# Performance work log

Measured on AMD Instinct MI355X. Metric: run time of the kernel, lower is better.

Reference implementation:

```python
import jax, jax.numpy as jnp
import numpy as np

B, S, D, H, F = 8, 1024, 512, 8, 2048
EPS = 1e-3  # keras default for BatchNormalization and LayerNormalization


def _layernorm(x, g, b):
    m = jnp.mean(x, axis=-1, keepdims=True)
    v = jnp.var(x, axis=-1, keepdims=True)
    return (x - m) * jax.lax.rsqrt(v + EPS) * g + b


def setup_inputs() -> dict:
    key = jax.random.key(0)
    ks = jax.random.split(key, 16)
    sc = 0.02
    inp = {
        "Q": jax.random.normal(ks[0], (B, S, D), jnp.float32),
        "K": jax.random.normal(ks[1], (B, S, D), jnp.float32),
        "V": jax.random.normal(ks[2], (B, S, D), jnp.float32),
        # per-head QKV projections stacked: [H, D, D]
        "WQ": jax.random.normal(ks[3], (H, D, D), jnp.float32) * sc,
        "bQ": jnp.zeros((H, D), jnp.float32),
        "WK": jax.random.normal(ks[4], (H, D, D), jnp.float32) * sc,
        "bK": jnp.zeros((H, D), jnp.float32),
        "WV": jax.random.normal(ks[5], (H, D, D), jnp.float32) * sc,
        "bV": jnp.zeros((H, D), jnp.float32),
        "Wo": jax.random.normal(ks[6], (H * D, D), jnp.float32) * sc,
        "bo": jnp.zeros((D,), jnp.float32),
        # FeedForward
        "W0": jax.random.normal(ks[7], (D, F), jnp.float32) * sc,
        "b0": jnp.zeros((F,), jnp.float32),
        "g0": jnp.ones((F,), jnp.float32),
        "be0": jnp.zeros((F,), jnp.float32),
        "m0": jnp.zeros((F,), jnp.float32),   # BN moving mean
        "v0": jnp.ones((F,), jnp.float32),    # BN moving var
        "a0": jnp.zeros((S, F), jnp.float32),  # PReLU alpha (keras default shape/init)
        "W1": jax.random.normal(ks[8], (F, F), jnp.float32) * sc,
        "b1": jnp.zeros((F,), jnp.float32),
        "g1": jnp.ones((F,), jnp.float32),
        "be1": jnp.zeros((F,), jnp.float32),
        "m1": jnp.zeros((F,), jnp.float32),
        "v1": jnp.ones((F,), jnp.float32),
        "a1": jnp.zeros((S, F), jnp.float32),
        "W2": jax.random.normal(ks[9], (F, D), jnp.float32) * sc,
        "b2": jnp.zeros((D,), jnp.float32),
        "ln0g": jnp.ones((D,), jnp.float32),
        "ln0b": jnp.zeros((D,), jnp.float32),
        "ln1g": jnp.ones((D,), jnp.float32),
        "ln1b": jnp.zeros((D,), jnp.float32),
    }
    return inp


def reference(Q, K, V, WQ, bQ, WK, bK, WV, bV, Wo, bo,
              W0, b0, g0, be0, m0, v0, a0,
              W1, b1, g1, be1, m1, v1, a1,
              W2, b2, ln0g, ln0b, ln1g, ln1b):
    # ---- MultiHeadAttention (all heads batched) ----
    qh = jnp.einsum('bsd,hde->bhse', Q, WQ) + bQ[None, :, None, :]
    kh = jnp.einsum('bsd,hde->bhse', K, WK) + bK[None, :, None, :]
    vh = jnp.einsum('bsd,hde->bhse', V, WV) + bV[None, :, None, :]
    # NOTE: source scales by 1/dk, not 1/sqrt(dk)
    scores = jnp.einsum('bhse,bhte->bhst', qh, kh) * (1.0 / D)
    attn = jax.nn.softmax(scores, axis=-1)
    ctx = jnp.einsum('bhst,bhte->bhse', attn, vh)        # [B,H,S,D]
    cat = jnp.transpose(ctx, (0, 2, 1, 3)).reshape(B, S, H * D)
    mha = cat @ Wo + bo
    x = _layernorm(Q + mha, ln0g, ln0b)
    # ---- FeedForward (inference: BN uses moving stats, dropout off) ----
    h0 = x @ W0 + b0
    h0 = (h0 - m0) * jax.lax.rsqrt(v0 + EPS) * g0 + be0
    h0 = jnp.where(h0 > 0, h0, a0 * h0)                   # PReLU
    h1 = h0 @ W1 + b1
    h1 = (h1 - m1) * jax.lax.rsqrt(v1 + EPS) * g1 + be1
    h1 = jnp.where(h1 > 0, h1, a1 * h1)
    ff = h1 @ W2 + b2
    return _layernorm(x + ff, ln1g, ln1b)
```

## Files before the change

### kernel.cpp

```cpp
#include <hip/hip_runtime.h>
#include <hip/hip_bf16.h>
#include <cstdint>
#include <cstddef>

#define Sd 1024
#define Dd 512
#define Hd 8
#define Fd 2048
#define Bd 8
#define EPSf 1e-3f

typedef __bf16 bf16x8 __attribute__((ext_vector_type(8)));
typedef float f32x4 __attribute__((ext_vector_type(4)));
typedef __attribute__((address_space(3))) unsigned int lds_u32;
typedef __attribute__((address_space(1))) const unsigned int gl_u32;

#define BM 128
#define BN 128
#define BK 32

enum { EPI_BF16 = 0, EPI_F32 = 1, EPI_BNPRELU = 2, EPI_SCORES = 3, EPI_PV = 4 };

__device__ __forceinline__ void gl_lds16(const void* g, void* l) {
  __builtin_amdgcn_global_load_lds((gl_u32*)g, (lds_u32*)l, 16, 0, 0);
}


#define LGKM(n)                                                  \
  asm volatile("s_waitcnt lgkmcnt(" #n ")" ::: "memory");        \
  __builtin_amdgcn_sched_barrier(0)
#define VMC(n) asm volatile("s_waitcnt vmcnt(" #n ")" ::: "memory")

#define LDA_(dst, dof, xr, mh)                                               \
  _Pragma("unroll") for (int i_ = 0; i_ < 4; ++i_)                           \
      dst[i_] = *(const bf16x8*)(aw + (dof) + (xr) + (mh) * 8192 + i_ * 2048);
#define LDB_(dst, dof, xr)                                                   \
  _Pragma("unroll") for (int i_ = 0; i_ < 4; ++i_)                           \
      dst[i_] = *(const bf16x8*)(bw + (dof) + (xr) + i_ * 2048);
#define MFMAQ(q, av, bv)                                                     \
  __builtin_amdgcn_s_setprio(1);                                             \
  {                                                                          \
    _Pragma("unroll") for (int i_ = 0; i_ < 4; ++i_) {                       \
      _Pragma("unroll") for (int n_ = 0; n_ < 4; ++n_)                       \
          acc[(q) * 4 + i_][n_] = __builtin_amdgcn_mfma_f32_16x16x32_bf16(   \
              av[i_], bv[n_], acc[(q) * 4 + i_][n_], 0, 0, 0);               \
    }                                                                        \
  }                                                                          \
  __builtin_amdgcn_s_setprio(0)

template <int EPI>
__global__ __launch_bounds__(512, 2) void big_gemm(
    const __hip_bfloat16* __restrict__ A_, int lda, size_t sA1, size_t sA2,
    const __hip_bfloat16* __restrict__ B_, size_t sB1,
    const float* __restrict__ bias_,
    void* __restrict__ C_, int ldc, size_t sC, int K, float alpha,
    const float* __restrict__ bn_g, const float* __restrict__ bn_b,
    const float* __restrict__ bn_m, const float* __restrict__ bn_v,
    const float* __restrict__ pa) {
  __shared__ __align__(16) char lds[131072];
  const int tid = threadIdx.x;
  const int gx = gridDim.x;
  const int nwg = gx * gridDim.y;
  const int orig = blockIdx.y * gx + blockIdx.x;
  const int wgid = (orig & 7) * (nwg >> 3) + (orig >> 3);
  const int bx = wgid % gx;
  const int by = wgid / gx;
  const int m0 = by * 256, n0 = bx * 256;
  const int z = blockIdx.z;
  const int z1 = z >> 3, z2 = z & 7;

  const int lane = tid & 63;
  const int wid = tid >> 6;
  const int wm = wid >> 2;
  const int wn = wid & 3;
  const int fr = lane & 15;
  const int kg = lane >> 4;

  const int r0 = tid >> 3;
  const int c0 = (tid & 7) ^ (r0 & 7);
  const size_t lda2 = (size_t)lda * 2;
  const size_t ldb2 = (size_t)K * 2;
  const char* Ab = (const char*)(A_ + (size_t)z1 * sA1 + (size_t)z2 * sA2) +
                   (size_t)(m0 + r0) * lda2 + c0 * 16;
  const char* Bb = (const char*)(B_ + (size_t)z1 * sB1) + (size_t)(n0 + r0) * ldb2 + c0 * 16;

  const int axor0 = (kg ^ (fr & 7)) << 4;
  const int axor1 = ((4 + kg) ^ (fr & 7)) << 4;
  const char* aw = lds + (wm << 14) + fr * 128;
  const char* bw = lds + 32768 + ((wn >> 1) << 14) + ((wn & 1) << 13) + fr * 128;

  auto STG = [&](int nof, int H, int u) {
    char* L = lds + nof + (H << 14) + tid * 16;
    const size_t rs = (H < 2) ? lda2 : ldb2;
    const char* src = ((H < 2) ? Ab : Bb) + (size_t)((H & 1) * 128) * rs + (size_t)u * 128;
    gl_lds16(src, L);
    gl_lds16(src + 64 * rs, L + 8192);
  };

  bf16x8 aA[4], aB[4], bA[4], bB[4];
  f32x4 acc[8][4] = {};
  const int NT = K >> 6;

  STG(0, 0, 0); STG(0, 1, 0); STG(0, 2, 0); STG(0, 3, 0);
  STG(65536, 0, 1); STG(65536, 1, 1); STG(65536, 2, 1); STG(65536, 3, 1);
  VMC(8);
  __builtin_amdgcn_s_barrier();
  LDA_(aA, 0, axor0, 0);
  LDB_(bA, 0, axor0);

  for (int u = 0; u < NT; ++u) {
    const int dof = (u & 1) << 16;
    const int nof = dof ^ 65536;
    const bool stg = (u >= 1) & (u + 1 < NT);
    LDA_(aB, dof, axor0, 1);
    if (stg) { STG(nof, 0, u + 1); STG(nof, 1, u + 1); }
    LGKM(4);
    MFMAQ(0, aA, bA);
    LDA_(aA, dof, axor1, 0);
    LDB_(bB, dof, axor1);
    if (stg) { STG(nof, 2, u + 1); STG(nof, 3, u + 1); }
    LGKM(8);
    MFMAQ(1, aB, bA);
    LDA_(aB, dof, axor1, 1);
    LGKM(4);
    MFMAQ(0, aA, bB);
    LGKM(0);
    if (u + 1 < NT) {
      VMC(0);
      __builtin_amdgcn_s_barrier();
      LDA_(aA, nof, axor0, 0);
      LDB_(bA, nof, axor0);
    }
    MFMAQ(1, aB, bB);
  }

  char* C = (char*)C_ + (size_t)z * sC * ((EPI == EPI_F32) ? 4 : 2);
  if (EPI == EPI_SCORES) {
    const float cvv = bn_m[z2];
    const float* ub = bn_g + (size_t)z2 * 8192 + (size_t)z1 * 1024;
    const float* wb = bn_b + (size_t)z2 * 8192 + (size_t)z1 * 1024;
    float* rs = (float*)bn_v + ((size_t)z << 10);
    float wc[4];
#pragma unroll
    for (int ni = 0; ni < 4; ++ni) wc[ni] = wb[n0 + wn * 64 + ni * 16 + fr];
#pragma unroll
    for (int mi = 0; mi < 8; ++mi) {
      const int rb = m0 + wm * 128 + mi * 16 + kg * 4;
      float rowa[4] = {0.f, 0.f, 0.f, 0.f};
#pragma unroll
      for (int ni = 0; ni < 4; ++ni) {
        const int col = n0 + wn * 64 + ni * 16 + fr;
#pragma unroll
        for (int j = 0; j < 4; ++j) {
          const int row = rb + j;
          const float e = __expf((acc[mi][ni][j] + ub[row] + wc[ni] + cvv) * alpha);
          rowa[j] += e;
          ((__hip_bfloat16*)C)[(size_t)row * ldc + col] = __float2bfloat16(e);
        }
      }
#pragma unroll
      for (int j = 0; j < 4; ++j) {
        float v = rowa[j];
        v += __shfl_xor(v, 1);
        v += __shfl_xor(v, 2);
        v += __shfl_xor(v, 4);
        v += __shfl_xor(v, 8);
        if (fr == 0) atomicAdd(rs + rb + j, v);
      }
    }
  } else {
#pragma unroll
    for (int ni = 0; ni < 4; ++ni) {
      const int col = n0 + wn * 64 + ni * 16 + fr;
      float bcol = 0.f, scale = 0.f, shift = 0.f;
      if (EPI != EPI_BF16) bcol = bias_[col];
      if (EPI == EPI_BNPRELU) {
        scale = bn_g[col] * rsqrtf(bn_v[col] + EPSf);
        shift = bn_b[col] - bn_m[col] * scale;
      }
#pragma unroll
      for (int mi = 0; mi < 8; ++mi) {
        const int rb = m0 + wm * 128 + mi * 16 + kg * 4;
#pragma unroll
        for (int j = 0; j < 4; ++j) {
          const int row = rb + j;
          float v = acc[mi][ni][j] * alpha + bcol;
          if (EPI == EPI_F32) {
            ((float*)C)[(size_t)row * ldc + col] = v;
          } else if (EPI == EPI_BF16) {
            ((__hip_bfloat16*)C)[(size_t)row * ldc + col] = __float2bfloat16(v);
          } else {
            v = v * scale + shift;
            const float aa = pa[(size_t)(row & (Sd - 1)) * Fd + col];
            v = v > 0.f ? v : aa * v;
            ((__hip_bfloat16*)C)[(size_t)row * ldc + col] = __float2bfloat16(v);
          }
        }
      }
    }
  }
}

template <int EPI>
__global__ __launch_bounds__(256, 2) void bt_gemm(
    const __hip_bfloat16* __restrict__ A_, int lda, size_t sA1, size_t sA2,
    const __hip_bfloat16* __restrict__ B_, int ldb, size_t sB1, size_t sB2,
    const float* __restrict__ bias_, size_t sBi1, size_t sBi2,
    void* __restrict__ C_, int ldc, size_t sC1, size_t sC2,
    int K, float alpha, int zshift,
    const float* __restrict__ bn_g, const float* __restrict__ bn_b,
    const float* __restrict__ bn_m, const float* __restrict__ bn_v,
    const float* __restrict__ pa) {
  __shared__ __hip_bfloat16 As[BM * BK];
  __shared__ __hip_bfloat16 Bs[BN * BK];

  const int tid = threadIdx.x;
  const int z = blockIdx.z;
  const int z1 = z >> zshift;
  const int z2 = z & ((1 << zshift) - 1);
  const int m0 = blockIdx.y * BM;
  const int n0 = blockIdx.x * BN;

  const __hip_bfloat16* A = A_ + (size_t)z1 * sA1 + (size_t)z2 * sA2;
  const __hip_bfloat16* Bt = B_ + (size_t)z1 * sB1 + (size_t)z2 * sB2;
  const float* bi = bias_ ? bias_ + (size_t)z1 * sBi1 + (size_t)z2 * sBi2 : nullptr;

  const int lane = tid & 63;
  const int wv = tid >> 6;
  const int wm = (wv >> 1) * 64;
  const int wn = (wv & 1) * 64;
  const int fr = lane & 15;
  const int kg = lane >> 4;

  const int srow = tid >> 2, sch = tid & 3;
  const size_t ldab = (size_t)lda * 2, ldbb = (size_t)ldb * 2;
  const char* Ap = (const char*)A + (size_t)(m0 + srow) * ldab + sch * 16;
  const char* Ap2 = Ap + 64 * ldab;
  const char* Bp = (const char*)Bt + (size_t)(n0 + srow) * ldbb + sch * 16;
  const char* Bp2 = Bp + 64 * ldbb;
  char* lA = (char*)As + tid * 16;
  char* lB = (char*)Bs + tid * 16;

  f32x4 acc[4][4] = {};

  for (int kt = 0; kt < K; kt += BK) {
    const size_t kb = (size_t)kt * 2;
    gl_lds16(Ap + kb, lA);
    gl_lds16(Ap2 + kb, lA + 4096);
    gl_lds16(Bp + kb, lB);
    gl_lds16(Bp2 + kb, lB + 4096);
    __syncthreads();

    bf16x8 afr[4], bfr[4];
#pragma unroll
    for (int mi = 0; mi < 4; ++mi)
      afr[mi] = *reinterpret_cast<const bf16x8*>(As + (wm + mi * 16 + fr) * BK + kg * 8);
#pragma unroll
    for (int ni = 0; ni < 4; ++ni)
      bfr[ni] = *reinterpret_cast<const bf16x8*>(Bs + (wn + ni * 16 + fr) * BK + kg * 8);
#pragma unroll
    for (int mi = 0; mi < 4; ++mi)
#pragma unroll
      for (int ni = 0; ni < 4; ++ni)
        acc[mi][ni] = __builtin_amdgcn_mfma_f32_16x16x32_bf16(afr[mi], bfr[ni], acc[mi][ni], 0, 0, 0);
    __syncthreads();
  }

  char* C = (char*)C_ + ((size_t)z1 * sC1 + (size_t)z2 * sC2) * ((EPI == EPI_F32) ? 4 : 2);
  float rinv_[4][4];
  if (EPI == EPI_PV) {
#pragma unroll
    for (int mi = 0; mi < 4; ++mi)
#pragma unroll
      for (int j = 0; j < 4; ++j)
        rinv_[mi][j] = 1.0f / bn_v[((size_t)z << 10) + m0 + wm + mi * 16 + kg * 4 + j];
  }
#pragma unroll
  for (int ni = 0; ni < 4; ++ni) {
    const int col = n0 + wn + ni * 16 + fr;
    float bcol = 0.f, scale = 0.f, shift = 0.f;
    if (bi) bcol = bi[col];
    if (EPI == EPI_BNPRELU) {
      scale = bn_g[col] * rsqrtf(bn_v[col] + EPSf);
      shift = bn_b[col] - bn_m[col] * scale;
    }
#pragma unroll
    for (int mi = 0; mi < 4; ++mi) {
      const int rb = m0 + wm + mi * 16 + kg * 4;
#pragma unroll
      for (int j = 0; j < 4; ++j) {
        const int row = rb + j;
        if (EPI == EPI_PV) {
          ((__hip_bfloat16*)C)[(size_t)row * ldc + col] = __float2bfloat16(acc[mi][ni][j] * rinv_[mi][j]);
        } else {
          float v = acc[mi][ni][j] * alpha + bcol;
          if (EPI == EPI_F32) {
            ((float*)C)[(size_t)row * ldc + col] = v;
          } else if (EPI == EPI_BF16) {
            ((__hip_bfloat16*)C)[(size_t)row * ldc + col] = __float2bfloat16(v);
          } else {
            v = v * scale + shift;
            const float a = pa[(size_t)(row & (Sd - 1)) * Fd + col];
            v = v > 0.f ? v : a * v;
            ((__hip_bfloat16*)C)[(size_t)row * ldc + col] = __float2bfloat16(v);
          }
        }
      }
    }
  }
}

__global__ __launch_bounds__(256) void tconv(const float* __restrict__ src,
                                             __hip_bfloat16* __restrict__ dst,
                                             int N, int Kfull, size_t sIn, size_t sOut) {
  __shared__ __hip_bfloat16 t[64][65];
  const float* s = src + (size_t)blockIdx.z * sIn;
  __hip_bfloat16* d = dst + (size_t)blockIdx.z * sOut;
  const int k0 = blockIdx.y * 64, n0 = blockIdx.x * 64;
  const int tid = threadIdx.x;
#pragma unroll
  for (int i = 0; i < 4; ++i) {
    int slot = tid + i * 256;
    int r = slot >> 4, c = (slot & 15) * 4;
    const float4 v = *reinterpret_cast<const float4*>(s + (size_t)(k0 + r) * N + n0 + c);
    t[c + 0][r] = __float2bfloat16(v.x);
    t[c + 1][r] = __float2bfloat16(v.y);
    t[c + 2][r] = __float2bfloat16(v.z);
    t[c + 3][r] = __float2bfloat16(v.w);
  }
  __syncthreads();
#pragma unroll
  for (int i = 0; i < 2; ++i) {
    int slot = tid + i * 256;
    int n = slot >> 3, kc = (slot & 7) * 8;
    __hip_bfloat16 tmp[8];
#pragma unroll
    for (int j = 0; j < 8; ++j) tmp[j] = t[n][kc + j];
    *reinterpret_cast<float4*>(d + (size_t)(n0 + n) * Kfull + k0 + kc) =
        *reinterpret_cast<const float4*>(tmp);
  }
}

__global__ __launch_bounds__(256) void conv3(const float* __restrict__ s0, const float* __restrict__ s1,
                                             const float* __restrict__ s2,
                                             __hip_bfloat16* __restrict__ d0, __hip_bfloat16* __restrict__ d1,
                                             __hip_bfloat16* __restrict__ d2) {
  const float* s = blockIdx.y == 0 ? s0 : (blockIdx.y == 1 ? s1 : s2);
  __hip_bfloat16* d = blockIdx.y == 0 ? d0 : (blockIdx.y == 1 ? d1 : d2);
  const size_t i = (size_t)blockIdx.x * 256 + threadIdx.x;
  const float4 a = reinterpret_cast<const float4*>(s)[2 * i];
  const float4 b = reinterpret_cast<const float4*>(s)[2 * i + 1];
  __hip_bfloat16 tmp[8] = {
      __float2bfloat16(a.x), __float2bfloat16(a.y), __float2bfloat16(a.z), __float2bfloat16(a.w),
      __float2bfloat16(b.x), __float2bfloat16(b.y), __float2bfloat16(b.z), __float2bfloat16(b.w)};
  *reinterpret_cast<float4*>(d + 8 * i) = *reinterpret_cast<const float4*>(tmp);
}

__device__ inline float wave_max(float v) {
#pragma unroll
  for (int o = 32; o > 0; o >>= 1) v = fmaxf(v, __shfl_xor(v, o));
  return v;
}
__device__ inline float wave_sum(float v) {
#pragma unroll
  for (int o = 32; o > 0; o >>= 1) v += __shfl_xor(v, o);
  return v;
}

__device__ inline float b2f(unsigned short u) {
  unsigned x = ((unsigned)u) << 16; float f; __builtin_memcpy(&f, &x, 4); return f;
}

__global__ __launch_bounds__(256) void tvec(const float* __restrict__ WQ, const float* __restrict__ bK,
                                            const float* __restrict__ WK, const float* __restrict__ bQ,
                                            float* __restrict__ t1, float* __restrict__ t2) {
  const float* W = blockIdx.y == 0 ? WQ : WK;
  const float* bb = blockIdx.y == 0 ? bK : bQ;
  float* out = blockIdx.y == 0 ? t1 : t2;
  const int wv = threadIdx.x >> 6, lane = threadIdx.x & 63;
  const int hd = blockIdx.x * 4 + wv;
  const int h = hd >> 9;
  float acc = 0.f;
#pragma unroll
  for (int j = 0; j < 8; ++j) {
    const int e = lane + 64 * j;
    acc += W[(size_t)hd * 512 + e] * bb[h * 512 + e];
  }
  acc = wave_sum(acc);
  if (lane == 0) out[hd] = acc;
}

__global__ __launch_bounds__(256) void uw_kernel(const float* __restrict__ Q, const float* __restrict__ K,
                                                 const float* __restrict__ t1, const float* __restrict__ t2,
                                                 float* __restrict__ u, float* __restrict__ w) {
  const int tid = threadIdx.x;
  const size_t row = blockIdx.x;
  const float2 q = reinterpret_cast<const float2*>(Q + row * 512)[tid];
  const float2 k = reinterpret_cast<const float2*>(K + row * 512)[tid];
  const int c = tid * 2;
  __shared__ float redu[8][4], redw[8][4];
  const int wv = tid >> 6;
#pragma unroll
  for (int h = 0; h < 8; ++h) {
    float ua = q.x * t1[h * 512 + c] + q.y * t1[h * 512 + c + 1];
    float wa = k.x * t2[h * 512 + c] + k.y * t2[h * 512 + c + 1];
    ua = wave_sum(ua);
    wa = wave_sum(wa);
    if ((tid & 63) == 0) { redu[h][wv] = ua; redw[h][wv] = wa; }
  }
  __syncthreads();
  if (tid < 8)
    u[tid * 8192 + row] = redu[tid][0] + redu[tid][1] + redu[tid][2] + redu[tid][3];
  else if (tid < 16)
    w[(tid - 8) * 8192 + row] = redw[tid - 8][0] + redw[tid - 8][1] + redw[tid - 8][2] + redw[tid - 8][3];
}

__global__ __launch_bounds__(256) void cvec(const float* __restrict__ bQ, const float* __restrict__ bK,
                                            float* __restrict__ c) {
  const int h = blockIdx.x, tid = threadIdx.x;
  const float2 a = reinterpret_cast<const float2*>(bQ + h * 512)[tid];
  const float2 b = reinterpret_cast<const float2*>(bK + h * 512)[tid];
  float acc = wave_sum(a.x * b.x + a.y * b.y);
  __shared__ float red[4];
  if ((tid & 63) == 0) red[tid >> 6] = acc;
  __syncthreads();
  if (tid == 0) c[h] = red[0] + red[1] + red[2] + red[3];
}

__global__ __launch_bounds__(256) void bvo_kernel(const __hip_bfloat16* __restrict__ wot,
                                                  const float* __restrict__ bV,
                                                  const float* __restrict__ bo,
                                                  float* __restrict__ bvo) {
  const int wv = threadIdx.x >> 6, lane = threadIdx.x & 63;
  const int e = blockIdx.x * 4 + wv;
  float acc = 0.f;
#pragma unroll
  for (int j = 0; j < 64; ++j) {
    const int hd = lane + 64 * j;
    acc += b2f(*(const unsigned short*)&wot[(size_t)e * 4096 + hd]) * bV[hd];
  }
  acc = wave_sum(acc);
  if (lane == 0) bvo[e] = bo[e] + acc;
}

__global__ __launch_bounds__(256) void add_ln3(const float* __restrict__ Xa, const float* __restrict__ Xb,
                                               const float* __restrict__ Xc, const float* __restrict__ cb,
                                               const float* __restrict__ gamma, const float* __restrict__ beta,
                                               float* __restrict__ out, __hip_bfloat16* __restrict__ outb) {
  const int tid = threadIdx.x;
  const size_t base = (size_t)blockIdx.x * Dd;
  const float2 a = reinterpret_cast<const float2*>(Xa + base)[tid];
  const float2 b = reinterpret_cast<const float2*>(Xb + base)[tid];
  const float2 c2 = reinterpret_cast<const float2*>(Xc + base)[tid];
  const int c = tid * 2;
  const float r0 = a.x + b.x + c2.x + cb[c];
  const float r1 = a.y + b.y + c2.y + cb[c + 1];
  float s = wave_sum(r0 + r1);
  float q = wave_sum(r0 * r0 + r1 * r1);
  __shared__ float rs[4], rq[4];
  if ((tid & 63) == 0) { rs[tid >> 6] = s; rq[tid >> 6] = q; }
  __syncthreads();
  const float mean = (rs[0] + rs[1] + rs[2] + rs[3]) * (1.f / Dd);
  const float msq = (rq[0] + rq[1] + rq[2] + rq[3]) * (1.f / Dd);
  const float inv = rsqrtf(msq - mean * mean + EPSf);
  const float y0 = (r0 - mean) * inv * gamma[c] + beta[c];
  const float y1 = (r1 - mean) * inv * gamma[c + 1] + beta[c + 1];
  out[base + c] = y0;
  out[base + c + 1] = y1;
  if (outb) {
    outb[base + c] = __float2bfloat16(y0);
    outb[base + c + 1] = __float2bfloat16(y1);
  }
}

extern "C" void kernel_launch(void* const* d_in, const int* in_sizes, int n_in,
                              void* d_out, int out_size, void* d_ws, size_t ws_size,
                              hipStream_t stream) {
  const float* Q = (const float*)d_in[0];
  const float* K = (const float*)d_in[1];
  const float* V = (const float*)d_in[2];
  const float* WQ = (const float*)d_in[3];
  const float* bQ = (const float*)d_in[4];
  const float* WK = (const float*)d_in[5];
  const float* bK = (const float*)d_in[6];
  const float* WV = (const float*)d_in[7];
  const float* bV = (const float*)d_in[8];
  const float* Wo = (const float*)d_in[9];
  const float* bo = (const float*)d_in[10];
  const float* W0 = (const float*)d_in[11];
  const float* b0 = (const float*)d_in[12];
  const float* g0 = (const float*)d_in[13];
  const float* be0 = (const float*)d_in[14];
  const float* m0 = (const float*)d_in[15];
  const float* v0 = (const float*)d_in[16];
  const float* a0 = (const float*)d_in[17];
  const float* W1 = (const float*)d_in[18];
  const float* b1 = (const float*)d_in[19];
  const float* g1 = (const float*)d_in[20];
  const float* be1 = (const float*)d_in[21];
  const float* m1 = (const float*)d_in[22];
  const float* v1 = (const float*)d_in[23];
  const float* a1 = (const float*)d_in[24];
  const float* W2 = (const float*)d_in[25];
  const float* b2 = (const float*)d_in[26];
  const float* ln0g = (const float*)d_in[27];
  const float* ln0b = (const float*)d_in[28];
  const float* ln1g = (const float*)d_in[29];
  const float* ln1b = (const float*)d_in[30];

  typedef __hip_bfloat16 bf;
  const size_t MB = 1u << 20;
  const size_t KB = 1u << 10;
  char* ws = (char*)d_ws;
  bf* PR = (bf*)(ws);
  bf* wot = (bf*)(ws + 64 * MB);
  bf* wqbf = (bf*)(ws + 68 * MB);
  bf* wkbf = (bf*)(ws + 72 * MB);
  bf* wvbf = (bf*)(ws + 76 * MB);
  bf* wqkt = (bf*)(ws + 80 * MB);
  bf* sc = (bf*)(ws + 64 * MB);
  bf* kbf = (bf*)(ws + 96 * MB);
  bf* vbft = (bf*)(ws + 104 * MB);
  bf* qbf = (bf*)(ws + 112 * MB);
  bf* wvot = (bf*)(ws + 112 * MB);
  float* u = (float*)(ws + 116 * MB);
  float* w = (float*)(ws + 116 * MB + 256 * KB);
  float* rsum = (float*)(ws + 116 * MB + 512 * KB);
  float* t1 = (float*)(ws + 116 * MB + 768 * KB);
  float* t2 = (float*)(ws + 116 * MB + 784 * KB);
  float* cv = (float*)(ws + 116 * MB + 800 * KB);
  float* bvo = (float*)(ws + 116 * MB + 804 * KB);
  float* mhap = (float*)(ws + 64 * MB);
  float* xbuf = (float*)(ws);
  bf* xb = (bf*)(ws + 16 * MB);
  bf* h0 = (bf*)(ws + 24 * MB);
  bf* h1 = (bf*)(ws + 56 * MB);
  float* ffp = (float*)(ws + 24 * MB);
  bf* w0t = (bf*)(ws + 96 * MB);
  bf* w1t = (bf*)(ws + 98 * MB);
  bf* w2t = (bf*)(ws + 106 * MB);

  const size_t SD = (size_t)Sd * Dd;
  const size_t DD = (size_t)Dd * Dd;
  const size_t SS = (size_t)Sd * Sd;
  const size_t SDH = (size_t)Sd * Hd * Dd;
  const float* np = nullptr;

  conv3<<<dim3(2048, 2), 256, 0, stream>>>(Q, K, K, qbf, kbf, kbf);
  conv3<<<dim3(1024, 3), 256, 0, stream>>>(WQ, WK, WV, wqbf, wkbf, wvbf);
  tconv<<<dim3(8, 16, 8), 256, 0, stream>>>(V, vbft, Dd, Sd, SD, SD);
  tconv<<<dim3(8, 64, 1), 256, 0, stream>>>(Wo, wot, Dd, Hd * Dd, 0, 0);

  bt_gemm<EPI_BF16><<<dim3(4, 4, 8), 256, 0, stream>>>(
      wkbf, Dd, 0, DD, wqbf, Dd, 0, DD, np, 0, 0,
      wqkt, Dd, 0, DD, Dd, 1.f, 3, np, np, np, np, np);
  big_gemm<EPI_BF16><<<dim3(16, 32, 1), 512, 0, stream>>>(
      qbf, Dd, 0, 0, wqkt, 0, np, PR, Hd * Dd, 0, Dd, 1.f, np, np, np, np, np);

  bt_gemm<EPI_BF16><<<dim3(4, 4, 8), 256, 0, stream>>>(
      wot, Hd * Dd, 0, 512, wvbf, Dd, 0, DD, np, 0, 0,
      wvot, Hd * Dd, 0, 512, Dd, 1.f, 3, np, np, np, np, np);
  tvec<<<dim3(1024, 2), 256, 0, stream>>>(WQ, bK, WK, bQ, t1, t2);
  uw_kernel<<<Bd * Sd, 256, 0, stream>>>(Q, K, t1, t2, u, w);
  cvec<<<8, 256, 0, stream>>>(bQ, bK, cv);
  bvo_kernel<<<128, 256, 0, stream>>>(wot, bV, bo, bvo);
  hipMemsetAsync(rsum, 0, 64 * 1024 * sizeof(float), stream);

  for (int bp = 0; bp < 4; ++bp) {
    const bf* Ap = PR + (size_t)bp * 2 * SDH;
    big_gemm<EPI_SCORES><<<dim3(4, 4, 16), 512, 0, stream>>>(
        Ap, Hd * Dd, SDH, 512, kbf + (size_t)bp * 2 * SD, SD, np,
        sc, Sd, SS, Dd, 1.f / (float)Dd,
        u + bp * 2048, w + bp * 2048, cv, rsum + bp * 16384, np);
    bt_gemm<EPI_PV><<<dim3(4, 8, 16), 256, 0, stream>>>(
        sc, Sd, 8 * SS, SS, vbft + (size_t)bp * 2 * SD, Sd, SD, 0, np, 0, 0,
        (void*)Ap, Hd * Dd, SDH, 512, Sd, 1.f, 3,
        np, np, np, rsum + bp * 16384, np);
  }

  bt_gemm<EPI_F32><<<dim3(4, 64, 2), 256, 0, stream>>>(
      PR, Hd * Dd, 2048, 0, wvot, Hd * Dd, 2048, 0, np, 0, 0,
      mhap, Dd, SDH, 0, 2048, 1.f, 0, np, np, np, np, np);
  add_ln3<<<Bd * Sd, 256, 0, stream>>>(Q, mhap, mhap + SDH, bvo, ln0g, ln0b, xbuf, xb);

  tconv<<<dim3(32, 8, 1), 256, 0, stream>>>(W0, w0t, Fd, Dd, 0, 0);
  tconv<<<dim3(32, 32, 1), 256, 0, stream>>>(W1, w1t, Fd, Fd, 0, 0);
  tconv<<<dim3(8, 32, 1), 256, 0, stream>>>(W2, w2t, Dd, Fd, 0, 0);

  big_gemm<EPI_BNPRELU><<<dim3(8, 32, 1), 512, 0, stream>>>(
      xb, Dd, 0, 0, w0t, 0, b0, h0, Fd, 0, Dd, 1.f, g0, be0, m0, v0, a0);
  big_gemm<EPI_BNPRELU><<<dim3(8, 32, 1), 512, 0, stream>>>(
      h0, Fd, 0, 0, w1t, 0, b1, h1, Fd, 0, Fd, 1.f, g1, be1, m1, v1, a1);
  bt_gemm<EPI_F32><<<dim3(4, 64, 2), 256, 0, stream>>>(
      h1, Fd, 1024, 0, w2t, Fd, 1024, 0, np, 0, 0,
      ffp, Dd, SDH, 0, 1024, 1.f, 0, np, np, np, np, np);
  add_ln3<<<Bd * Sd, 256, 0, stream>>>(xbuf, ffp, ffp + SDH, b2, ln1g, ln1b, (float*)d_out, nullptr);
}
```

Before: 662.2 us.

## Fuse scores, exp and PV into a single flash-style attention kernel

Replaces the per-batch-pair loop of a scores GEMM (writing bf16 exp-scores to global memory) followed by a PV GEMM with one fused kernel. Each block keeps a 32-row Q tile in LDS, computes 128-column score tiles, exponentiates into LDS, accumulates row sums in shared memory and multiplies by V in-register, then normalizes and writes the context in place. This removes the large score-matrix round trip through global memory, the rsum memset and several launches. In exchange, K and V are read directly from global memory without LDS staging, the blocks are smaller, and the per-tile barriers may limit MFMA throughput.

```diff
diff --git a/kernel.cpp b/kernel.cpp
--- a/kernel.cpp
+++ b/kernel.cpp
@@ -19,12 +19,140 @@
 #define BN 128
 #define BK 32
 
-enum { EPI_BF16 = 0, EPI_F32 = 1, EPI_BNPRELU = 2, EPI_SCORES = 3, EPI_PV = 4 };
+enum { EPI_BF16 = 0, EPI_F32 = 1, EPI_BNPRELU = 2 };
 
 __device__ __forceinline__ void gl_lds16(const void* g, void* l) {
   __builtin_amdgcn_global_load_lds((gl_u32*)g, (lds_u32*)l, 16, 0, 0);
 }
-
+__device__ inline unsigned short f2b_(float f) {
+  __hip_bfloat16 h = __float2bfloat16(f); unsigned short s; __builtin_memcpy(&s, &h, 2); return s;
+}
+
+__global__ __launch_bounds__(512, 4) void attn_fused(
+    __hip_bfloat16* __restrict__ P,
+    const __hip_bfloat16* __restrict__ Kb,
+    const __hip_bfloat16* __restrict__ Vt,
+    const float* __restrict__ u, const float* __restrict__ w,
+    const float* __restrict__ cv) {
+  __shared__ __align__(16) char ldsA[32768];
+  __shared__ __align__(16) char ldsS[8192];
+  __shared__ float rsum[32];
+  const int tid = threadIdx.x;
+  const int id = blockIdx.x + 32 * blockIdx.y;
+  const int xcd = id & 7, slot = id >> 3;
+  const int z = xcd + 8 * (slot >> 5);
+  const int m0 = (slot & 31) * 32;
+  const int b = z >> 3, h = z & 7;
+
+  const int lane = tid & 63, wid = tid >> 6;
+  const int fr = lane & 15, kg = lane >> 4;
+  const int mS = wid >> 2, nS = wid & 3;
+
+#pragma unroll
+  for (int p = 0; p < 4; ++p) {
+    const int s = p * 512 + tid;
+    const int r = s >> 6, c = s & 63;
+    const int sc_ = (c & ~7) | ((c & 7) ^ (r & 7));
+    gl_lds16((const char*)P + ((size_t)(b * 1024 + m0 + r)) * 8192 + h * 1024 + sc_ * 16,
+             ldsA + s * 16);
+  }
+  if (tid < 32) rsum[tid] = 0.f;
+  __syncthreads();
+
+  const float cvh = cv[h];
+  const float* us = u + h * 8192 + b * 1024 + m0;
+  const float* wsb = w + h * 8192 + b * 1024;
+  const char* Kbase = (const char*)Kb + (size_t)b * 1048576;
+  const char* Vbase = (const char*)Vt + (size_t)b * 1048576;
+  const char* aRow = ldsA + (mS * 16 + fr) * 1024;
+  const float alpha = 1.f / (float)Dd;
+
+  f32x4 O[2][4] = {};
+
+  for (int t = 0; t < 8; ++t) {
+    const int t0 = t * 128;
+    f32x4 Sacc[2] = {};
+    const char* kRow = Kbase + (size_t)(t0 + nS * 32 + fr) * 1024 + kg * 16;
+    bf16x8 kf0 = *(const bf16x8*)(kRow);
+    bf16x8 kf1 = *(const bf16x8*)(kRow + 16384);
+#pragma unroll
+    for (int ks = 0; ks < 16; ++ks) {
+      bf16x8 kn0, kn1;
+      if (ks + 1 < 16) {
+        kn0 = *(const bf16x8*)(kRow + (ks + 1) * 64);
+        kn1 = *(const bf16x8*)(kRow + 16384 + (ks + 1) * 64);
+      }
+      const int c = ks * 4 + kg;
+      const int sc_ = (c & ~7) | ((c & 7) ^ (fr & 7));
+      const bf16x8 af = *(const bf16x8*)(aRow + sc_ * 16);
+      Sacc[0] = __builtin_amdgcn_mfma_f32_16x16x32_bf16(af, kf0, Sacc[0], 0, 0, 0);
+      Sacc[1] = __builtin_amdgcn_mfma_f32_16x16x32_bf16(af, kf1, Sacc[1], 0, 0, 0);
+      kf0 = kn0; kf1 = kn1;
+    }
+    float part[4] = {0.f, 0.f, 0.f, 0.f};
+#pragma unroll
+    for (int ni = 0; ni < 2; ++ni) {
+      const int tl = nS * 32 + ni * 16 + fr;
+      const float wv_ = wsb[t0 + tl];
+      const int chb = tl >> 3;
+#pragma unroll
+      for (int j = 0; j < 4; ++j) {
+        const int rl = mS * 16 + kg * 4 + j;
+        const float e = __expf((Sacc[ni][j] + us[rl] + wv_ + cvh) * alpha);
+        part[j] += e;
+        const int ch = (chb & ~7) | ((chb & 7) ^ (rl & 7));
+        *(unsigned short*)(ldsS + rl * 256 + ch * 16 + (tl & 7) * 2) = f2b_(e);
+      }
+    }
+#pragma unroll
+    for (int j = 0; j < 4; ++j) {
+      float v = part[j];
+      v += __shfl_xor(v, 1); v += __shfl_xor(v, 2);
+      v += __shfl_xor(v, 4); v += __shfl_xor(v, 8);
+      if (fr == 0) atomicAdd(&rsum[mS * 16 + kg * 4 + j], v);
+    }
+    __syncthreads();
+#pragma unroll
+    for (int ks = 0; ks < 4; ++ks) {
+      bf16x8 vf[4];
+#pragma unroll
+      for (int ni = 0; ni < 4; ++ni)
+        vf[ni] = *(const bf16x8*)(Vbase + (size_t)(wid * 64 + ni * 16 + fr) * 2048 +
+                                  (size_t)t0 * 2 + ks * 64 + kg * 16);
+      bf16x8 sa[2];
+#pragma unroll
+      for (int mi = 0; mi < 2; ++mi) {
+        const int c = ks * 4 + kg;
+        const int ch = (c & ~7) | ((c & 7) ^ (fr & 7));
+        sa[mi] = *(const bf16x8*)(ldsS + (mi * 16 + fr) * 256 + ch * 16);
+      }
+#pragma unroll
+      for (int mi = 0; mi < 2; ++mi)
+#pragma unroll
+        for (int ni = 0; ni < 4; ++ni)
+          O[mi][ni] = __builtin_amdgcn_mfma_f32_16x16x32_bf16(sa[mi], vf[ni], O[mi][ni], 0, 0, 0);
+    }
+    __syncthreads();
+  }
+
+  float rinv[2][4];
+#pragma unroll
+  for (int mi = 0; mi < 2; ++mi)
+#pragma unroll
+    for (int j = 0; j < 4; ++j)
+      rinv[mi][j] = 1.f / rsum[mi * 16 + kg * 4 + j];
+#pragma unroll
+  for (int mi = 0; mi < 2; ++mi)
+#pragma unroll
+    for (int ni = 0; ni < 4; ++ni) {
+      const int col = h * 512 + wid * 64 + ni * 16 + fr;
+#pragma unroll
+      for (int j = 0; j < 4; ++j) {
+        const size_t row = (size_t)b * 1024 + m0 + mi * 16 + kg * 4 + j;
+        P[row * 4096 + col] = __float2bfloat16(O[mi][ni][j] * rinv[mi][j]);
+      }
+    }
+}
 
 #define LGKM(n)                                                  \
   asm volatile("s_waitcnt lgkmcnt(" #n ")" ::: "memory");        \
@@ -135,66 +263,31 @@
   }
 
   char* C = (char*)C_ + (size_t)z * sC * ((EPI == EPI_F32) ? 4 : 2);
-  if (EPI == EPI_SCORES) {
-    const float cvv = bn_m[z2];
-    const float* ub = bn_g + (size_t)z2 * 8192 + (size_t)z1 * 1024;
-    const float* wb = bn_b + (size_t)z2 * 8192 + (size_t)z1 * 1024;
-    float* rs = (float*)bn_v + ((size_t)z << 10);
-    float wc[4];
-#pragma unroll
-    for (int ni = 0; ni < 4; ++ni) wc[ni] = wb[n0 + wn * 64 + ni * 16 + fr];
+#pragma unroll
+  for (int ni = 0; ni < 4; ++ni) {
+    const int col = n0 + wn * 64 + ni * 16 + fr;
+    float bcol = 0.f, scale = 0.f, shift = 0.f;
+    if (EPI != EPI_BF16) bcol = bias_[col];
+    if (EPI == EPI_BNPRELU) {
+      scale = bn_g[col] * rsqrtf(bn_v[col] + EPSf);
+      shift = bn_b[col] - bn_m[col] * scale;
+    }
 #pragma unroll
     for (int mi = 0; mi < 8; ++mi) {
       const int rb = m0 + wm * 128 + mi * 16 + kg * 4;
-      float rowa[4] = {0.f, 0.f, 0.f, 0.f};
-#pragma unroll
-      for (int ni = 0; ni < 4; ++ni) {
-        const int col = n0 + wn * 64 + ni * 16 + fr;
-#pragma unroll
-        for (int j = 0; j < 4; ++j) {
-          const int row = rb + j;
-          const float e = __expf((acc[mi][ni][j] + ub[row] + wc[ni] + cvv) * alpha);
-          rowa[j] += e;
-          ((__hip_bfloat16*)C)[(size_t)row * ldc + col] = __float2bfloat16(e);
-        }
-      }
 #pragma unroll
       for (int j = 0; j < 4; ++j) {
-        float v = rowa[j];
-        v += __shfl_xor(v, 1);
-        v += __shfl_xor(v, 2);
-        v += __shfl_xor(v, 4);
-        v += __shfl_xor(v, 8);
-        if (fr == 0) atomicAdd(rs + rb + j, v);
-      }
-    }
-  } else {
-#pragma unroll
-    for (int ni = 0; ni < 4; ++ni) {
-      const int col = n0 + wn * 64 + ni * 16 + fr;
-      float bcol = 0.f, scale = 0.f, shift = 0.f;
-      if (EPI != EPI_BF16) bcol = bias_[col];
-      if (EPI == EPI_BNPRELU) {
-        scale = bn_g[col] * rsqrtf(bn_v[col] + EPSf);
-        shift = bn_b[col] - bn_m[col] * scale;
-      }
-#pragma unroll
-      for (int mi = 0; mi < 8; ++mi) {
-        const int rb = m0 + wm * 128 + mi * 16 + kg * 4;
-#pragma unroll
-        for (int j = 0; j < 4; ++j) {
-          const int row = rb + j;
-          float v = acc[mi][ni][j] * alpha + bcol;
-          if (EPI == EPI_F32) {
-            ((float*)C)[(size_t)row * ldc + col] = v;
-          } else if (EPI == EPI_BF16) {
-            ((__hip_bfloat16*)C)[(size_t)row * ldc + col] = __float2bfloat16(v);
-          } else {
-            v = v * scale + shift;
-            const float aa = pa[(size_t)(row & (Sd - 1)) * Fd + col];
-            v = v > 0.f ? v : aa * v;
-            ((__hip_bfloat16*)C)[(size_t)row * ldc + col] = __float2bfloat16(v);
-          }
+        const int row = rb + j;
+        float v = acc[mi][ni][j] * alpha + bcol;
+        if (EPI == EPI_F32) {
+          ((float*)C)[(size_t)row * ldc + col] = v;
+        } else if (EPI == EPI_BF16) {
+          ((__hip_bfloat16*)C)[(size_t)row * ldc + col] = __float2bfloat16(v);
+        } else {
+          v = v * scale + shift;
+          const float aa = pa[(size_t)(row & (Sd - 1)) * Fd + col];
+          v = v > 0.f ? v : aa * v;
+          ((__hip_bfloat16*)C)[(size_t)row * ldc + col] = __float2bfloat16(v);
         }
       }
     }
@@ -267,14 +360,6 @@
   }
 
   char* C = (char*)C_ + ((size_t)z1 * sC1 + (size_t)z2 * sC2) * ((EPI == EPI_F32) ? 4 : 2);
-  float rinv_[4][4];
-  if (EPI == EPI_PV) {
-#pragma unroll
-    for (int mi = 0; mi < 4; ++mi)
-#pragma unroll
-      for (int j = 0; j < 4; ++j)
-        rinv_[mi][j] = 1.0f / bn_v[((size_t)z << 10) + m0 + wm + mi * 16 + kg * 4 + j];
-  }
 #pragma unroll
   for (int ni = 0; ni < 4; ++ni) {
     const int col = n0 + wn + ni * 16 + fr;
@@ -290,20 +375,16 @@
 #pragma unroll
       for (int j = 0; j < 4; ++j) {
         const int row = rb + j;
-        if (EPI == EPI_PV) {
-          ((__hip_bfloat16*)C)[(size_t)row * ldc + col] = __float2bfloat16(acc[mi][ni][j] * rinv_[mi][j]);
+        float v = acc[mi][ni][j] * alpha + bcol;
+        if (EPI == EPI_F32) {
+          ((float*)C)[(size_t)row * ldc + col] = v;
+        } else if (EPI == EPI_BF16) {
+          ((__hip_bfloat16*)C)[(size_t)row * ldc + col] = __float2bfloat16(v);
         } else {
-          float v = acc[mi][ni][j] * alpha + bcol;
-          if (EPI == EPI_F32) {
-            ((float*)C)[(size_t)row * ldc + col] = v;
-          } else if (EPI == EPI_BF16) {
-            ((__hip_bfloat16*)C)[(size_t)row * ldc + col] = __float2bfloat16(v);
-          } else {
-            v = v * scale + shift;
-            const float a = pa[(size_t)(row & (Sd - 1)) * Fd + col];
-            v = v > 0.f ? v : a * v;
-            ((__hip_bfloat16*)C)[(size_t)row * ldc + col] = __float2bfloat16(v);
-          }
+          v = v * scale + shift;
+          const float a = pa[(size_t)(row & (Sd - 1)) * Fd + col];
+          v = v > 0.f ? v : a * v;
+          ((__hip_bfloat16*)C)[(size_t)row * ldc + col] = __float2bfloat16(v);
         }
       }
     }
@@ -356,11 +437,6 @@
   *reinterpret_cast<float4*>(d + 8 * i) = *reinterpret_cast<const float4*>(tmp);
 }
 
-__device__ inline float wave_max(float v) {
-#pragma unroll
-  for (int o = 32; o > 0; o >>= 1) v = fmaxf(v, __shfl_xor(v, o));
-  return v;
-}
 __device__ inline float wave_sum(float v) {
 #pragma unroll
   for (int o = 32; o > 0; o >>= 1) v += __shfl_xor(v, o);
@@ -518,14 +594,12 @@
   bf* wkbf = (bf*)(ws + 72 * MB);
   bf* wvbf = (bf*)(ws + 76 * MB);
   bf* wqkt = (bf*)(ws + 80 * MB);
-  bf* sc = (bf*)(ws + 64 * MB);
   bf* kbf = (bf*)(ws + 96 * MB);
   bf* vbft = (bf*)(ws + 104 * MB);
   bf* qbf = (bf*)(ws + 112 * MB);
   bf* wvot = (bf*)(ws + 112 * MB);
   float* u = (float*)(ws + 116 * MB);
   float* w = (float*)(ws + 116 * MB + 256 * KB);
-  float* rsum = (float*)(ws + 116 * MB + 512 * KB);
   float* t1 = (float*)(ws + 116 * MB + 768 * KB);
   float* t2 = (float*)(ws + 116 * MB + 784 * KB);
   float* cv = (float*)(ws + 116 * MB + 800 * KB);
@@ -542,7 +616,6 @@
 
   const size_t SD = (size_t)Sd * Dd;
   const size_t DD = (size_t)Dd * Dd;
-  const size_t SS = (size_t)Sd * Sd;
   const size_t SDH = (size_t)Sd * Hd * Dd;
   const float* np = nullptr;
 
@@ -564,19 +637,8 @@
   uw_kernel<<<Bd * Sd, 256, 0, stream>>>(Q, K, t1, t2, u, w);
   cvec<<<8, 256, 0, stream>>>(bQ, bK, cv);
   bvo_kernel<<<128, 256, 0, stream>>>(wot, bV, bo, bvo);
-  hipMemsetAsync(rsum, 0, 64 * 1024 * sizeof(float), stream);
-
-  for (int bp = 0; bp < 4; ++bp) {
-    const bf* Ap = PR + (size_t)bp * 2 * SDH;
-    big_gemm<EPI_SCORES><<<dim3(4, 4, 16), 512, 0, stream>>>(
-        Ap, Hd * Dd, SDH, 512, kbf + (size_t)bp * 2 * SD, SD, np,
-        sc, Sd, SS, Dd, 1.f / (float)Dd,
-        u + bp * 2048, w + bp * 2048, cv, rsum + bp * 16384, np);
-    bt_gemm<EPI_PV><<<dim3(4, 8, 16), 256, 0, stream>>>(
-        sc, Sd, 8 * SS, SS, vbft + (size_t)bp * 2 * SD, Sd, SD, 0, np, 0, 0,
-        (void*)Ap, Hd * Dd, SDH, 512, Sd, 1.f, 3,
-        np, np, np, rsum + bp * 16384, np);
-  }
+
+  attn_fused<<<dim3(32, 64), 512, 0, stream>>>(PR, kbf, vbft, u, w, cv);
 
   bt_gemm<EPI_F32><<<dim3(4, 64, 2), 256, 0, stream>>>(
       PR, Hd * Dd, 2048, 0, wvot, Hd * Dd, 2048, 0, np, 0, 0,
```

New measurement: 1.113 ms. 68.1% more time.
